# Optimization experiments

Measured on AMD Instinct MI355X. Metric: run time of the kernel, lower is better.

The kernel has to match this reference:

```python
import jax, jax.numpy as jnp
import numpy as np

V, E, H, F_IN, F_OUT, F_E = 30000, 500000, 4, 32, 32, 32
NEG_SLOPE = 0.2

def _act(x):
    return jax.nn.leaky_relu(x, NEG_SLOPE)

def setup_inputs() -> dict:
    key = jax.random.key(0)
    ks = jax.random.split(key, 24)
    def lin(kw, kb, fin, fout):
        W = jax.random.normal(kw, (fin, fout), jnp.float32) * (1.0 / np.sqrt(fin))
        b = jax.random.normal(kb, (fout,), jnp.float32) * 0.01
        return W, b
    W_as, b_as = lin(ks[0], ks[1], F_IN, F_IN)
    W_ad, b_ad = lin(ks[2], ks[3], F_IN, F_IN)
    W_ae, b_ae = lin(ks[4], ks[5], F_E, F_IN)
    W_dot, b_dot = lin(ks[6], ks[7], F_IN, 1)
    W_ms, b_ms = lin(ks[8], ks[9], F_IN, F_OUT)
    W_md, b_md = lin(ks[10], ks[11], F_IN, F_OUT)
    W_me, b_me = lin(ks[12], ks[13], F_E, F_OUT)
    W_wn, b_wn = lin(ks[14], ks[15], F_IN, F_OUT)
    node_feats = jax.random.normal(ks[16], (V, H, F_IN), jnp.float32)
    edge_feats = jax.random.normal(ks[17], (E, F_E), jnp.float32)
    src_idx = jax.random.randint(ks[18], (E,), 0, V, jnp.int32)
    dst_idx = jax.random.randint(ks[19], (E,), 0, V, jnp.int32)
    return {
        'node_feats': node_feats, 'edge_feats': edge_feats,
        'src_idx': src_idx, 'dst_idx': dst_idx,
        'W_as': W_as, 'b_as': b_as, 'W_ad': W_ad, 'b_ad': b_ad,
        'W_ae': W_ae, 'b_ae': b_ae, 'W_dot': W_dot, 'b_dot': b_dot,
        'W_ms': W_ms, 'b_ms': b_ms, 'W_md': W_md, 'b_md': b_md,
        'W_me': W_me, 'b_me': b_me, 'W_wn': W_wn, 'b_wn': b_wn,
    }

def reference(node_feats, edge_feats, src_idx, dst_idx,
              W_as, b_as, W_ad, b_ad, W_ae, b_ae, W_dot, b_dot,
              W_ms, b_ms, W_md, b_md, W_me, b_me, W_wn, b_wn):
    n_nodes = node_feats.shape[0]
    # attention path
    src = node_feats @ W_as + b_as                      # (V,H,F)
    dst = node_feats @ W_ad + b_ad                      # (V,H,F)
    edg_atn = (edge_feats @ W_ae + b_ae)[:, None, :]    # (E,1,F)
    e = _act(src[src_idx] + dst[dst_idx] + edg_atn)     # (E,H,F)
    scores = e @ W_dot + b_dot                          # (E,H,1)
    # edge softmax: normalize over incoming edges of each dst node
    smax = jax.ops.segment_max(scores, dst_idx, num_segments=n_nodes)
    ex = jnp.exp(scores - smax[dst_idx])
    ssum = jax.ops.segment_sum(ex, dst_idx, num_segments=n_nodes)
    alpha = ex / ssum[dst_idx]                          # (E,H,1)
    # message path
    msg_s = node_feats @ W_ms + b_ms                    # (V,H,Fo)
    msg_d = node_feats @ W_md + b_md                    # (V,H,Fo)
    msg_e = (edge_feats @ W_me + b_me)[:, None, :]      # (E,1,Fo)
    atn_inp = _act(msg_s[src_idx] + msg_d[dst_idx] + msg_e)  # (E,H,Fo)
    feat = jax.ops.segment_sum(alpha * atn_inp, dst_idx, num_segments=n_nodes)  # (V,H,Fo)
    out = _act(feat + node_feats @ W_wn + b_wn)         # (V,H,Fo)
    return out
```

## Files before the change

kernel.cpp:

```cpp
#include <hip/hip_runtime.h>
#include <hip/hip_bf16.h>

#define V_N 30000
#define E_N 500000
#define XW  512
#define HB  1954

typedef __attribute__((ext_vector_type(8))) short bf16x8;
typedef __attribute__((ext_vector_type(4))) float f32x4;

__device__ __forceinline__ float lrelu(float x) { return fmaxf(x, 0.2f * x); }
__device__ __forceinline__ unsigned short f2bf(float f) {
    __hip_bfloat16 h = __float2bfloat16(f);
    return *reinterpret_cast<unsigned short*>(&h);
}
__device__ __forceinline__ float bf_lo(unsigned u) { return __uint_as_float(u << 16); }
__device__ __forceinline__ float bf_hi(unsigned u) { return __uint_as_float(u & 0xffff0000u); }

template<int CTRL, int RMASK>
__device__ __forceinline__ float dpp_add(float t) {
    int b = __builtin_amdgcn_update_dpp(0, __float_as_int(t), CTRL, RMASK, 0xF, true);
    return t + __int_as_float(b);
}

__device__ __forceinline__ float group_sum(float t, int lane) {
    t = dpp_add<0x121, 0xF>(t);
    t = dpp_add<0x122, 0xF>(t);
    t = dpp_add<0x124, 0xF>(t);
    t = dpp_add<0x128, 0xF>(t);
    t = dpp_add<0x142, 0xA>(t);
    float u = __shfl_xor(t, 16);
    return (lane & 16) ? t : u;
}

__global__ __launch_bounds__(256) void xform_hist_mfma(
    const float* __restrict__ nf,
    const float* __restrict__ Was, const float* __restrict__ bas,
    const float* __restrict__ Wms, const float* __restrict__ bms,
    const float* __restrict__ Wad, const float* __restrict__ bad,
    const float* __restrict__ Wmd, const float* __restrict__ bmd,
    const int* __restrict__ dst,
    uint4* __restrict__ tab_s, uint4* __restrict__ tab_d, int* __restrict__ deg)
{
    int tid = threadIdx.x;
    if (blockIdx.x >= XW) {
        int i = (blockIdx.x - XW) * 256 + tid;
        if (i < E_N) atomicAdd(&deg[dst[i]], 1);
        return;
    }
    int lane = tid & 63;
    int l15 = lane & 15, q = lane >> 4;
    bf16x8 Bas0, Bas1, Bad0, Bad1, Bms0, Bms1, Bmd0, Bmd1;
    #pragma unroll
    for (int i = 0; i < 8; ++i) {
        int k = q * 8 + i;
        Bas0[i] = (short)f2bf(Was[k * 32 + l15]);
        Bas1[i] = (short)f2bf(Was[k * 32 + 16 + l15]);
        Bad0[i] = (short)f2bf(Wad[k * 32 + l15]);
        Bad1[i] = (short)f2bf(Wad[k * 32 + 16 + l15]);
        Bms0[i] = (short)f2bf(Wms[k * 32 + l15]);
        Bms1[i] = (short)f2bf(Wms[k * 32 + 16 + l15]);
        Bmd0[i] = (short)f2bf(Wmd[k * 32 + l15]);
        Bmd1[i] = (short)f2bf(Wmd[k * 32 + 16 + l15]);
    }
    float bs0 = bas[l15], bs1 = bas[16 + l15];
    float bd0 = bad[l15], bd1 = bad[16 + l15];
    float bm0 = bms[l15], bm1 = bms[16 + l15];
    float bn0 = bmd[l15], bn1 = bmd[16 + l15];

    int wv = tid >> 6;
    const int ntiles = V_N / 4;
    for (int tile = blockIdx.x * 4 + wv; tile < ntiles; tile += XW * 4) {
        int nbase = tile * 4;
        int rbase = nbase * 4;
        const float4* ap = (const float4*)(nf + (size_t)(rbase + l15) * 32 + q * 8);
        float4 a0 = ap[0], a1 = ap[1];
        bf16x8 A;
        A[0] = (short)f2bf(a0.x); A[1] = (short)f2bf(a0.y);
        A[2] = (short)f2bf(a0.z); A[3] = (short)f2bf(a0.w);
        A[4] = (short)f2bf(a1.x); A[5] = (short)f2bf(a1.y);
        A[6] = (short)f2bf(a1.z); A[7] = (short)f2bf(a1.w);
        f32x4 z = {0.f, 0.f, 0.f, 0.f};
        f32x4 Das0 = __builtin_amdgcn_mfma_f32_16x16x32_bf16(A, Bas0, z, 0, 0, 0);
        f32x4 Das1 = __builtin_amdgcn_mfma_f32_16x16x32_bf16(A, Bas1, z, 0, 0, 0);
        f32x4 Dad0 = __builtin_amdgcn_mfma_f32_16x16x32_bf16(A, Bad0, z, 0, 0, 0);
        f32x4 Dad1 = __builtin_amdgcn_mfma_f32_16x16x32_bf16(A, Bad1, z, 0, 0, 0);
        f32x4 Dms0 = __builtin_amdgcn_mfma_f32_16x16x32_bf16(A, Bms0, z, 0, 0, 0);
        f32x4 Dms1 = __builtin_amdgcn_mfma_f32_16x16x32_bf16(A, Bms1, z, 0, 0, 0);
        f32x4 Dmd0 = __builtin_amdgcn_mfma_f32_16x16x32_bf16(A, Bmd0, z, 0, 0, 0);
        f32x4 Dmd1 = __builtin_amdgcn_mfma_f32_16x16x32_bf16(A, Bmd1, z, 0, 0, 0);
        int node = nbase + q;
        uint4 lo, hi;
        lo.x = f2bf(Das0[0] + bs0) | ((unsigned)f2bf(Das0[1] + bs0) << 16);
        lo.y = f2bf(Das0[2] + bs0) | ((unsigned)f2bf(Das0[3] + bs0) << 16);
        lo.z = f2bf(Dms0[0] + bm0) | ((unsigned)f2bf(Dms0[1] + bm0) << 16);
        lo.w = f2bf(Dms0[2] + bm0) | ((unsigned)f2bf(Dms0[3] + bm0) << 16);
        hi.x = f2bf(Das1[0] + bs1) | ((unsigned)f2bf(Das1[1] + bs1) << 16);
        hi.y = f2bf(Das1[2] + bs1) | ((unsigned)f2bf(Das1[3] + bs1) << 16);
        hi.z = f2bf(Dms1[0] + bm1) | ((unsigned)f2bf(Dms1[1] + bm1) << 16);
        hi.w = f2bf(Dms1[2] + bm1) | ((unsigned)f2bf(Dms1[3] + bm1) << 16);
        tab_s[(size_t)node * 32 + l15]      = lo;
        tab_s[(size_t)node * 32 + 16 + l15] = hi;
        uint4 lod, hid;
        lod.x = f2bf(Dad0[0] + bd0) | ((unsigned)f2bf(Dad0[1] + bd0) << 16);
        lod.y = f2bf(Dad0[2] + bd0) | ((unsigned)f2bf(Dad0[3] + bd0) << 16);
        lod.z = f2bf(Dmd0[0] + bn0) | ((unsigned)f2bf(Dmd0[1] + bn0) << 16);
        lod.w = f2bf(Dmd0[2] + bn0) | ((unsigned)f2bf(Dmd0[3] + bn0) << 16);
        hid.x = f2bf(Dad1[0] + bd1) | ((unsigned)f2bf(Dad1[1] + bd1) << 16);
        hid.y = f2bf(Dad1[2] + bd1) | ((unsigned)f2bf(Dad1[3] + bd1) << 16);
        hid.z = f2bf(Dmd1[0] + bn1) | ((unsigned)f2bf(Dmd1[1] + bn1) << 16);
        hid.w = f2bf(Dmd1[2] + bn1) | ((unsigned)f2bf(Dmd1[3] + bn1) << 16);
        tab_d[(size_t)node * 32 + l15]      = lod;
        tab_d[(size_t)node * 32 + 16 + l15] = hid;
    }
}

__global__ __launch_bounds__(1024) void scan_k(
    const int* __restrict__ deg, int* __restrict__ rowptr, int* __restrict__ cursor)
{
    __shared__ int wsum[16];
    __shared__ int carry_s;
    int tid = threadIdx.x;
    int lane = tid & 63, wv = tid >> 6;
    if (tid == 0) carry_s = 0;
    __syncthreads();
    for (int base = 0; base < V_N; base += 1024) {
        int i = base + tid;
        int v = (i < V_N) ? deg[i] : 0;
        int x = v;
        #pragma unroll
        for (int off = 1; off < 64; off <<= 1) {
            int t = __shfl_up(x, off, 64);
            if (lane >= off) x += t;
        }
        if (lane == 63) wsum[wv] = x;
        __syncthreads();
        if (wv == 0 && lane < 16) {
            int s = wsum[lane];
            #pragma unroll
            for (int off = 1; off < 16; off <<= 1) {
                int t = __shfl_up(s, off, 64);
                if (lane >= off) s += t;
            }
            wsum[lane] = s;
        }
        __syncthreads();
        int woff  = (wv == 0) ? 0 : wsum[wv - 1];
        int carry = carry_s;
        int excl  = carry + woff + x - v;
        if (i < V_N) { rowptr[i] = excl; cursor[i] = excl; }
        __syncthreads();
        if (tid == 1023) carry_s = carry + wsum[15];
        __syncthreads();
    }
    if (tid == 0) rowptr[V_N] = carry_s;
}

__global__ __launch_bounds__(256) void scatter_k(
    const int* __restrict__ dst, const int* __restrict__ src,
    int* __restrict__ cursor, int* __restrict__ pos, int* __restrict__ csr_src)
{
    int i = blockIdx.x * 256 + threadIdx.x;
    if (i < E_N) {
        int p = atomicAdd(&cursor[dst[i]], 1);
        pos[i] = p;
        csr_src[p] = src[i];
    }
}

__global__ __launch_bounds__(256) void edge_gemv_mfma(
    const float* __restrict__ ef, const int* __restrict__ pos,
    const float* __restrict__ Wae, const float* __restrict__ bae,
    const float* __restrict__ Wme, const float* __restrict__ bme,
    unsigned* __restrict__ em)
{
    int tid  = threadIdx.x;
    int lane = tid & 63;
    int l15  = lane & 15, q = lane >> 4;
    bf16x8 B0, B1, B2, B3;
    #pragma unroll
    for (int i = 0; i < 8; ++i) {
        int k = q * 8 + i;
        B0[i] = (short)f2bf(Wae[k * 32 + l15]);
        B1[i] = (short)f2bf(Wae[k * 32 + 16 + l15]);
        B2[i] = (short)f2bf(Wme[k * 32 + l15]);
        B3[i] = (short)f2bf(Wme[k * 32 + 16 + l15]);
    }
    float ba0 = bae[l15], ba1 = bae[16 + l15];
    float bm0 = bme[l15], bm1 = bme[16 + l15];

    int wid = (blockIdx.x * 256 + tid) >> 6;
    int nw  = (gridDim.x * 256) >> 6;
    const int ntiles = E_N / 16;
    for (int tile = wid; tile < ntiles; tile += nw) {
        int ebase = tile * 16;
        const float4* ap = (const float4*)(ef + (size_t)(ebase + l15) * 32 + q * 8);
        float4 a0 = ap[0], a1 = ap[1];
        int pv = pos[ebase + l15];
        bf16x8 A;
        A[0] = (short)f2bf(a0.x); A[1] = (short)f2bf(a0.y);
        A[2] = (short)f2bf(a0.z); A[3] = (short)f2bf(a0.w);
        A[4] = (short)f2bf(a1.x); A[5] = (short)f2bf(a1.y);
        A[6] = (short)f2bf(a1.z); A[7] = (short)f2bf(a1.w);
        f32x4 z = {0.f, 0.f, 0.f, 0.f};
        f32x4 D0 = __builtin_amdgcn_mfma_f32_16x16x32_bf16(A, B0, z, 0, 0, 0);
        f32x4 D1 = __builtin_amdgcn_mfma_f32_16x16x32_bf16(A, B1, z, 0, 0, 0);
        f32x4 D2 = __builtin_amdgcn_mfma_f32_16x16x32_bf16(A, B2, z, 0, 0, 0);
        f32x4 D3 = __builtin_amdgcn_mfma_f32_16x16x32_bf16(A, B3, z, 0, 0, 0);
        #pragma unroll
        for (int j = 0; j < 4; ++j) {
            int r = q * 4 + j;
            int p = __shfl(pv, r, 64);
            unsigned lo = f2bf(D0[j] + ba0) | ((unsigned)f2bf(D2[j] + bm0) << 16);
            unsigned hi = f2bf(D1[j] + ba1) | ((unsigned)f2bf(D3[j] + bm1) << 16);
            em[(size_t)p * 32 + l15]      = lo;
            em[(size_t)p * 32 + 16 + l15] = hi;
        }
    }
}

__global__ __launch_bounds__(256) void node_gather4(
    const int* __restrict__ rowptr, const int* __restrict__ csr_src,
    const unsigned* __restrict__ em, const uint4* __restrict__ tab_s,
    const uint4* __restrict__ tab_d,
    const float* __restrict__ Wdot,
    const float* __restrict__ Wwn, const float* __restrict__ bwn,
    const float* __restrict__ nf,
    float* __restrict__ out)
{
    __shared__ float ww[1024], wd[32];
    int tid = threadIdx.x;
    for (int i = tid; i < 1024; i += 256) ww[i] = Wwn[i];
    if (tid < 32) wd[tid] = Wdot[tid] * 1.4426950408889634f;
    __syncthreads();
    int lane = tid & 31;
    int n = blockIdx.x * 8 + (tid >> 5);
    float wdl = wd[lane];

    float da[4], dm[4];
    {
        uint4 v = tab_d[(size_t)n * 32 + lane];
        da[0] = bf_lo(v.x); da[1] = bf_hi(v.x);
        da[2] = bf_lo(v.y); da[3] = bf_hi(v.y);
        dm[0] = bf_lo(v.z); dm[1] = bf_hi(v.z);
        dm[2] = bf_lo(v.w); dm[3] = bf_hi(v.w);
    }

    float acc0 = 0.f, acc1 = 0.f, acc2 = 0.f, acc3 = 0.f;
    float s0 = 0.f, s1 = 0.f, s2 = 0.f, s3 = 0.f;
    int p0 = rowptr[n], p1 = rowptr[n + 1];

    uint4 gc = make_uint4(0, 0, 0, 0);
    unsigned ec = 0;
    if (p0 < p1) {
        int si = csr_src[p0];
        gc = tab_s[(size_t)si * 32 + lane];
        ec = em[(size_t)p0 * 32 + lane];
    }
    for (int p = p0; p < p1; ++p) {
        uint4 g = gc; unsigned ev = ec;
        if (p + 1 < p1) {
            int sn = csr_src[p + 1];
            gc = tab_s[(size_t)sn * 32 + lane];
            ec = em[(size_t)(p + 1) * 32 + lane];
        }
        float ea = bf_lo(ev), me = bf_hi(ev);
        float t0 = lrelu(bf_lo(g.x) + da[0] + ea) * wdl;
        float t1 = lrelu(bf_hi(g.x) + da[1] + ea) * wdl;
        float t2 = lrelu(bf_lo(g.y) + da[2] + ea) * wdl;
        float t3 = lrelu(bf_hi(g.y) + da[3] + ea) * wdl;
        t0 = group_sum(t0, lane);
        t1 = group_sum(t1, lane);
        t2 = group_sum(t2, lane);
        t3 = group_sum(t3, lane);
        float x0 = exp2f(t0), x1 = exp2f(t1);
        float x2 = exp2f(t2), x3 = exp2f(t3);
        float m0 = lrelu(bf_lo(g.z) + dm[0] + me);
        float m1 = lrelu(bf_hi(g.z) + dm[1] + me);
        float m2 = lrelu(bf_lo(g.w) + dm[2] + me);
        float m3 = lrelu(bf_hi(g.w) + dm[3] + me);
        acc0 = fmaf(x0, m0, acc0); s0 += x0;
        acc1 = fmaf(x1, m1, acc1); s1 += x1;
        acc2 = fmaf(x2, m2, acc2); s2 += x2;
        acc3 = fmaf(x3, m3, acc3); s3 += x3;
    }
    #pragma unroll
    for (int h = 0; h < 4; ++h) {
        float x = nf[(size_t)n * 128 + h * 32 + lane];
        float a = bwn[lane];
        #pragma unroll
        for (int k = 0; k < 32; ++k)
            a = fmaf(__shfl(x, k, 32), ww[k * 32 + lane], a);
        float accv = (h == 0) ? acc0 : (h == 1) ? acc1 : (h == 2) ? acc2 : acc3;
        float sv   = (h == 0) ? s0   : (h == 1) ? s1   : (h == 2) ? s2   : s3;
        float f = (sv > 0.f) ? accv / sv : 0.f;
        out[(size_t)n * 128 + h * 32 + lane] = lrelu(f + a);
    }
}

extern "C" void kernel_launch(void* const* d_in, const int* in_sizes, int n_in,
                              void* d_out, int out_size, void* d_ws, size_t ws_size,
                              hipStream_t stream)
{
    const float* nf  = (const float*)d_in[0];
    const float* ef  = (const float*)d_in[1];
    const int*   src = (const int*)d_in[2];
    const int*   dst = (const int*)d_in[3];
    const float* Was = (const float*)d_in[4],  *bas = (const float*)d_in[5];
    const float* Wad = (const float*)d_in[6],  *bad = (const float*)d_in[7];
    const float* Wae = (const float*)d_in[8],  *bae = (const float*)d_in[9];
    const float* Wdot= (const float*)d_in[10];
    const float* Wms = (const float*)d_in[12], *bms = (const float*)d_in[13];
    const float* Wmd = (const float*)d_in[14], *bmd = (const float*)d_in[15];
    const float* Wme = (const float*)d_in[16], *bme = (const float*)d_in[17];
    const float* Wwn = (const float*)d_in[18], *bwn = (const float*)d_in[19];

    const size_t em_w  = (size_t)E_N * 32;
    const size_t tab_w = (size_t)V_N * 32;
    unsigned* em     = (unsigned*)d_ws;
    uint4*    tab_s  = (uint4*)(em + em_w);
    uint4*    tab_d  = tab_s + tab_w;
    int*      deg    = (int*)(tab_d + tab_w);
    int*      rowptr = deg + V_N;
    int*      cursor = rowptr + V_N + 1;
    int*      pos    = cursor + V_N;
    int*      csr_src= pos + E_N;

    hipMemsetAsync(deg, 0, V_N * sizeof(int), stream);

    const int ebk = (E_N + 255) / 256;

    xform_hist_mfma<<<XW + HB, 256, 0, stream>>>(nf, Was, bas, Wms, bms,
                                                 Wad, bad, Wmd, bmd, dst,
                                                 tab_s, tab_d, deg);
    scan_k<<<1, 1024, 0, stream>>>(deg, rowptr, cursor);
    scatter_k<<<ebk, 256, 0, stream>>>(dst, src, cursor, pos, csr_src);
    edge_gemv_mfma<<<2048, 256, 0, stream>>>(ef, pos, Wae, bae, Wme, bme, em);
    node_gather4<<<3750, 256, 0, stream>>>(rowptr, csr_src, em, tab_s, tab_d,
                                           Wdot, Wwn, bwn, nf, (float*)d_out);
}
```

Before: 187.2 us.

## Sort nodes by in-degree into a permutation to balance gather warp work

Adds a degree histogram to the scan kernel and a new kernel that bucket-sorts node ids by descending in-degree into a permutation array. The gather kernel then maps each 32-lane group to perm[...] instead of its linear node id, so groups within a block handle nodes of similar degree and divergence on the per-node edge loop drops. This costs an extra kernel launch, global atomics on 128 bin counters, and an indirect lookup that scatters tab_d, nf and out accesses across nodes instead of keeping them contiguous.

```diff
diff --git a/kernel.cpp b/kernel.cpp
--- a/kernel.cpp
+++ b/kernel.cpp
@@ -116,13 +116,16 @@
 }
 
 __global__ __launch_bounds__(1024) void scan_k(
-    const int* __restrict__ deg, int* __restrict__ rowptr, int* __restrict__ cursor)
+    const int* __restrict__ deg, int* __restrict__ rowptr, int* __restrict__ cursor,
+    int* __restrict__ bincur)
 {
     __shared__ int wsum[16];
     __shared__ int carry_s;
+    __shared__ int bh[128];
     int tid = threadIdx.x;
     int lane = tid & 63, wv = tid >> 6;
     if (tid == 0) carry_s = 0;
+    if (tid < 128) bh[tid] = 0;
     __syncthreads();
     for (int base = 0; base < V_N; base += 1024) {
         int i = base + tid;
@@ -148,12 +151,30 @@
         int woff  = (wv == 0) ? 0 : wsum[wv - 1];
         int carry = carry_s;
         int excl  = carry + woff + x - v;
-        if (i < V_N) { rowptr[i] = excl; cursor[i] = excl; }
+        if (i < V_N) {
+            rowptr[i] = excl; cursor[i] = excl;
+            atomicAdd(&bh[min(v, 127)], 1);
+        }
         __syncthreads();
         if (tid == 1023) carry_s = carry + wsum[15];
         __syncthreads();
     }
-    if (tid == 0) rowptr[V_N] = carry_s;
+    if (tid == 0) {
+        rowptr[V_N] = carry_s;
+        int off = 0;
+        for (int b = 127; b >= 0; --b) { bincur[b] = off; off += bh[b]; }
+    }
+}
+
+__global__ __launch_bounds__(256) void perm_k(
+    const int* __restrict__ deg, int* __restrict__ bincur, int* __restrict__ perm)
+{
+    int i = blockIdx.x * 256 + threadIdx.x;
+    if (i < V_N) {
+        int b = min(deg[i], 127);
+        int p = atomicAdd(&bincur[b], 1);
+        perm[p] = i;
+    }
 }
 
 __global__ __launch_bounds__(256) void scatter_k(
@@ -226,6 +247,7 @@
     const float* __restrict__ Wdot,
     const float* __restrict__ Wwn, const float* __restrict__ bwn,
     const float* __restrict__ nf,
+    const int* __restrict__ perm,
     float* __restrict__ out)
 {
     __shared__ float ww[1024], wd[32];
@@ -234,7 +256,7 @@
     if (tid < 32) wd[tid] = Wdot[tid] * 1.4426950408889634f;
     __syncthreads();
     int lane = tid & 31;
-    int n = blockIdx.x * 8 + (tid >> 5);
+    int n = perm[blockIdx.x * 8 + (tid >> 5)];
     float wdl = wd[lane];
 
     float da[4], dm[4];
@@ -325,17 +347,21 @@
     int*      cursor = rowptr + V_N + 1;
     int*      pos    = cursor + V_N;
     int*      csr_src= pos + E_N;
+    int*      bincur = csr_src + E_N;
+    int*      perm   = bincur + 128;
 
     hipMemsetAsync(deg, 0, V_N * sizeof(int), stream);
 
     const int ebk = (E_N + 255) / 256;
+    const int pbk = (V_N + 255) / 256;
 
     xform_hist_mfma<<<XW + HB, 256, 0, stream>>>(nf, Was, bas, Wms, bms,
                                                  Wad, bad, Wmd, bmd, dst,
                                                  tab_s, tab_d, deg);
-    scan_k<<<1, 1024, 0, stream>>>(deg, rowptr, cursor);
+    scan_k<<<1, 1024, 0, stream>>>(deg, rowptr, cursor, bincur);
+    perm_k<<<pbk, 256, 0, stream>>>(deg, bincur, perm);
     scatter_k<<<ebk, 256, 0, stream>>>(dst, src, cursor, pos, csr_src);
     edge_gemv_mfma<<<2048, 256, 0, stream>>>(ef, pos, Wae, bae, Wme, bme, em);
     node_gather4<<<3750, 256, 0, stream>>>(rowptr, csr_src, em, tab_s, tab_d,
-                                           Wdot, Wwn, bwn, nf, (float*)d_out);
-}
+                                           Wdot, Wwn, bwn, nf, perm, (float*)d_out);
+}
```

Measured after the change: 256.1 us. 36.9% more time.
